# Kernel optimization log

Measured on AMD Instinct MI355X. Metric: run time of the kernel, lower is better.

Reference implementation:

```python
import jax, jax.numpy as jnp
import numpy as np
import math

N_EMBD = 768
N_HEAD = 12
B, T = 4, 1024


def setup_inputs() -> dict:
    key = jax.random.key(0)
    ks = jax.random.split(key, 12)
    s = 0.02
    d = N_EMBD
    inp = {
        'x': jax.random.normal(ks[0], (B, T, d), dtype=jnp.float32),
        'refractory_state': jax.random.uniform(ks[1], (B, T), dtype=jnp.float32),
        'ln1_w': jnp.ones((d,), jnp.float32),
        'ln1_b': jnp.zeros((d,), jnp.float32),
        'c_attn_w': jax.random.normal(ks[2], (d, 3 * d), dtype=jnp.float32) * s,
        'c_attn_b': jnp.zeros((3 * d,), jnp.float32),
        'c_proj_w': jax.random.normal(ks[3], (d, d), dtype=jnp.float32) * s,
        'c_proj_b': jnp.zeros((d,), jnp.float32),
        'threshold': jnp.full((N_HEAD,), 0.01, jnp.float32),
        'leak': jnp.full((N_HEAD,), 2.0, jnp.float32),
        'steepness': jnp.full((N_HEAD,), 2.0, jnp.float32),
        'refractory_strength': jnp.full((N_HEAD,), -2.0, jnp.float32),
        'cross_layer_weight': jnp.full((N_HEAD,), -2.0, jnp.float32),
        'ln2_w': jnp.ones((d,), jnp.float32),
        'ln2_b': jnp.zeros((d,), jnp.float32),
        'fc_w': jax.random.normal(ks[4], (d, 4 * d), dtype=jnp.float32) * s,
        'fc_b': jnp.zeros((4 * d,), jnp.float32),
        'proj_w': jax.random.normal(ks[5], (4 * d, d), dtype=jnp.float32) * s,
        'proj_b': jnp.zeros((d,), jnp.float32),
    }
    return inp


def _layer_norm(x, w, b, eps=1e-5):
    m = jnp.mean(x, axis=-1, keepdims=True)
    v = jnp.var(x, axis=-1, keepdims=True)
    return (x - m) * jax.lax.rsqrt(v + eps) * w + b


def _per_head(p):
    # [H] -> [1, H, 1, 1]
    return p.reshape(1, -1, 1, 1)


def ember_block(x, refractory_state, ln1_w, ln1_b, c_attn_w, c_attn_b,
                c_proj_w, c_proj_b, threshold, leak, steepness,
                refractory_strength, cross_layer_weight,
                ln2_w, ln2_b, fc_w, fc_b, proj_w, proj_b):
    Bx, Tx, C = x.shape
    hd = C // N_HEAD

    h = _layer_norm(x, ln1_w, ln1_b)
    qkv = h @ c_attn_w + c_attn_b
    q, k, v = jnp.split(qkv, 3, axis=-1)
    # [B, T, C] -> [B, H, T, hd]
    q = q.reshape(Bx, Tx, N_HEAD, hd).transpose(0, 2, 1, 3)
    k = k.reshape(Bx, Tx, N_HEAD, hd).transpose(0, 2, 1, 3)
    v = v.reshape(Bx, Tx, N_HEAD, hd).transpose(0, 2, 1, 3)

    att = jnp.einsum('bhqd,bhkd->bhqk', q, k) * (1.0 / math.sqrt(hd))
    causal = jnp.tril(jnp.ones((Tx, Tx), dtype=bool))
    att = jnp.where(causal, att, -jnp.inf)
    att_probs = jax.nn.softmax(att, axis=-1)

    # per-head LIF modulation with refractory dynamics
    thr = jnp.abs(_per_head(threshold)) * 0.1
    lk = jax.nn.sigmoid(_per_head(leak))
    stp = jax.nn.softplus(_per_head(steepness))

    column_load = att_probs.mean(axis=-2, keepdims=True)  # [B,H,1,T]
    ref_strength = jax.nn.softplus(_per_head(refractory_strength))
    eff_thr = thr + ref_strength * column_load
    cross_w = jax.nn.sigmoid(_per_head(cross_layer_weight))
    prev_load = refractory_state[:, None, None, :]  # [B,1,1,T]
    eff_thr = eff_thr + cross_w * prev_load

    fire_mask = jax.nn.sigmoid(stp * (att_probs - eff_thr))
    lif_weights = fire_mask + lk * (1.0 - fire_mask)
    modulated = att_probs * lif_weights
    modulated = modulated / (modulated.sum(axis=-1, keepdims=True) + 1e-8)
    new_refractory = modulated.mean(axis=1).mean(axis=-2)  # [B,T]

    y = jnp.einsum('bhqk,bhkd->bhqd', modulated, v)
    y = y.transpose(0, 2, 1, 3).reshape(Bx, Tx, C)
    y = y @ c_proj_w + c_proj_b
    x = x + y

    # MLP
    h2 = _layer_norm(x, ln2_w, ln2_b)
    h2 = jax.nn.gelu(h2 @ fc_w + fc_b, approximate=False)
    h2 = h2 @ proj_w + proj_b
    x = x + h2
    return x, new_refractory


def reference(x, refractory_state, ln1_w, ln1_b, c_attn_w, c_attn_b,
              c_proj_w, c_proj_b, threshold, leak, steepness,
              refractory_strength, cross_layer_weight,
              ln2_w, ln2_b, fc_w, fc_b, proj_w, proj_b):
    return ember_block(x, refractory_state, ln1_w, ln1_b, c_attn_w, c_attn_b,
                       c_proj_w, c_proj_b, threshold, leak, steepness,
                       refractory_strength, cross_layer_weight,
                       ln2_w, ln2_b, fc_w, fc_b, proj_w, proj_b)
```

## Files before the change

### kernel.cpp

```cpp
#include <hip/hip_runtime.h>
#include <hip/hip_bf16.h>
#include <math.h>

typedef unsigned short ushort;
typedef __attribute__((ext_vector_type(8))) unsigned short ushort8;
typedef __attribute__((ext_vector_type(8))) short s16x8;
typedef __attribute__((ext_vector_type(4))) float f32x4;

constexpr int NE = 768;
constexpr int NH = 12;
constexpr int HD = 64;
constexpr int Bc = 4;
constexpr int Tc = 1024;
constexpr int BT = Bc * Tc;

__device__ __forceinline__ ushort f2bf(float f) {
    __hip_bfloat16 h = __float2bfloat16(f);
    return *reinterpret_cast<ushort*>(&h);
}
__device__ __forceinline__ float bf2f(ushort u) {
    return __uint_as_float(((unsigned)u) << 16);
}
__device__ __forceinline__ float softplus_f(float x) {
    return (x > 20.f) ? x : log1pf(__expf(x));
}
__device__ __forceinline__ float rcp_f(float x) {
#if __has_builtin(__builtin_amdgcn_rcpf)
    return __builtin_amdgcn_rcpf(x);
#else
    return 1.f / x;
#endif
}
__device__ __forceinline__ void gload16(const void* g, void* l) {
    __builtin_amdgcn_global_load_lds((const __attribute__((address_space(1))) void*)g,
                                     (__attribute__((address_space(3))) void*)l, 16, 0, 0);
}

__device__ __forceinline__ void ln_row(const float* __restrict__ x,
                                       const float* __restrict__ w,
                                       const float* __restrict__ b,
                                       ushort* __restrict__ out, int row, int t) {
    const float* xr = x + (size_t)row * NE;
    float v0 = xr[t], v1 = xr[t + 256], v2 = xr[t + 512];
    float s = v0 + v1 + v2;
    float s2 = v0 * v0 + v1 * v1 + v2 * v2;
#pragma unroll
    for (int o = 32; o > 0; o >>= 1) {
        s += __shfl_xor(s, o);
        s2 += __shfl_xor(s2, o);
    }
    __shared__ float lws[4], lws2[4];
    int wv = t >> 6;
    if ((t & 63) == 0) { lws[wv] = s; lws2[wv] = s2; }
    __syncthreads();
    float sum = lws[0] + lws[1] + lws[2] + lws[3];
    float sq = lws2[0] + lws2[1] + lws2[2] + lws2[3];
    float mean = sum * (1.0f / NE);
    float var = sq * (1.0f / NE) - mean * mean;
    float rs = rsqrtf(var + 1e-5f);
    ushort* orow = out + (size_t)row * NE;
    orow[t]       = f2bf((v0 - mean) * rs * w[t]       + b[t]);
    orow[t + 256] = f2bf((v1 - mean) * rs * w[t + 256] + b[t + 256]);
    orow[t + 512] = f2bf((v2 - mean) * rs * w[t + 512] + b[t + 512]);
}

__global__ __launch_bounds__(256) void ln_kernel(const float* __restrict__ x,
                                                 const float* __restrict__ w,
                                                 const float* __restrict__ b,
                                                 ushort* __restrict__ out) {
    ln_row(x, w, b, out, blockIdx.x, threadIdx.x);
}

__device__ __forceinline__ void wconv_tile(const float* __restrict__ W,
                                           ushort* __restrict__ Wt,
                                           int K, int N, int bx, int by, int tid) {
    __shared__ float t[32][33];
    int n0 = bx * 32, k0 = by * 32;
    int c = tid & 31, r4 = tid >> 5;
#pragma unroll
    for (int i = 0; i < 4; ++i) {
        int r = r4 + i * 8;
        t[r][c] = W[(size_t)(k0 + r) * N + n0 + c];
    }
    __syncthreads();
#pragma unroll
    for (int i = 0; i < 4; ++i) {
        int r = r4 + i * 8;
        Wt[(size_t)(n0 + r) * K + k0 + c] = f2bf(t[c][r]);
    }
}

__global__ __launch_bounds__(256) void wconvert_all(
    const float* __restrict__ Wa, ushort* __restrict__ Ta,
    const float* __restrict__ Wc, ushort* __restrict__ Tcp,
    const float* __restrict__ Wf, ushort* __restrict__ Tf,
    const float* __restrict__ Wp, ushort* __restrict__ Tp,
    float* __restrict__ colsum, float* __restrict__ refr_out,
    const float* __restrict__ x, const float* __restrict__ ln1_w,
    const float* __restrict__ ln1_b, ushort* __restrict__ hbuf) {
    int blk = blockIdx.x, tid = threadIdx.x;
    if (blk >= 6964) {
        ln_row(x, ln1_w, ln1_b, hbuf, blk - 6964, tid);
        return;
    }
    if (blk >= 6912) {
        int i = (blk - 6912) * 256 + tid;
        float4 z = make_float4(0.f, 0.f, 0.f, 0.f);
        if (i < 12288) ((float4*)colsum)[i] = z;
        else ((float4*)refr_out)[i - 12288] = z;
        return;
    }
    if (blk < 1728) {
        wconv_tile(Wa, Ta, 768, 2304, blk % 72, blk / 72, tid);
    } else if (blk < 2304) {
        int i = blk - 1728;
        wconv_tile(Wc, Tcp, 768, 768, i % 24, i / 24, tid);
    } else if (blk < 4608) {
        int i = blk - 2304;
        wconv_tile(Wf, Tf, 768, 3072, i % 96, i / 96, tid);
    } else {
        int i = blk - 4608;
        wconv_tile(Wp, Tp, 3072, 768, i % 24, i / 24, tid);
    }
}

template <int BM, int BN, int OUT_MODE, int ACT, bool RES>
__global__ __launch_bounds__(256) void mfma_gemm(
    const ushort* __restrict__ A, const ushort* __restrict__ Bt,
    const float* __restrict__ bias, const float* __restrict__ residual,
    float* __restrict__ Cf, ushort* __restrict__ Cb,
    ushort* __restrict__ Qo, ushort* __restrict__ Ko, ushort* __restrict__ Vo,
    int M, int N, int K, int NBX, int KLD, int NSPLIT) {
    constexpr int NF = (BM == 128) ? 4 : 2;
    constexpr int MF = (BM == 64 && BN == 64) ? 2 : 4;
    constexpr int WN = BN / (NF * 16);
    constexpr int APASS = BM / 32, BPASS = BN / 32;
    constexpr bool DBUF = (BM == 64 && BN == 64);
    constexpr int NBUF = DBUF ? 2 : 1;
    __shared__ __align__(16) ushort As[NBUF * BM * 64];
    __shared__ __align__(16) ushort Bs[NBUF * BN * 64];
    int tid = threadIdx.x;
    int lane = tid & 63;
    int nb = gridDim.x;
    int lin = blockIdx.x;
    int nl = (lin & 7) * (nb >> 3) + (lin >> 3);
    int nper = nb / NSPLIT;
    int sp = nl / nper;
    int rem2 = nl - sp * nper;
    int bx = rem2 % NBX, by = rem2 / NBX;
    int m0 = by * BM, n0 = bx * BN;
    int kbase = sp * K;
    int wave = tid >> 6;
    int wr = wave / WN, wc = wave % WN;
    f32x4 acc[MF][NF] = {};
    int srow = tid >> 3;
    int scol = (tid & 7) ^ (srow & 7);
    const ushort* ga = A + (size_t)(m0 + srow) * KLD + kbase + scol * 8;
    const ushort* gb = Bt + (size_t)(n0 + srow) * KLD + kbase + scol * 8;
    char* lA = (char*)As + tid * 16;
    char* lB = (char*)Bs + tid * 16;
    int fr = lane & 15, g = lane >> 4;
    unsigned swz = (unsigned)((fr & 7) << 4);
    const char* abase = (const char*)As + (wr * (MF * 16) + fr) * 128;
    const char* bbase = (const char*)Bs + (wc * (NF * 16) + fr) * 128;

    if constexpr (DBUF) {
        constexpr int ABYTES = BM * 64 * 2, BBYTES = BN * 64 * 2;
        int nk = K >> 6;
#pragma unroll
        for (int p = 0; p < APASS; ++p) gload16(ga + (size_t)(p * 32) * KLD, lA + p * 4096);
#pragma unroll
        for (int p = 0; p < BPASS; ++p) gload16(gb + (size_t)(p * 32) * KLD, lB + p * 4096);
        for (int k = 0; k < nk; ++k) {
            int cur = k & 1;
            if (k + 1 < nk) {
                int nxt = cur ^ 1;
                int k0 = (k + 1) << 6;
#pragma unroll
                for (int p = 0; p < APASS; ++p)
                    gload16(ga + (size_t)(p * 32) * KLD + k0, lA + nxt * ABYTES + p * 4096);
#pragma unroll
                for (int p = 0; p < BPASS; ++p)
                    gload16(gb + (size_t)(p * 32) * KLD + k0, lB + nxt * BBYTES + p * 4096);
                asm volatile("s_waitcnt vmcnt(4)" ::: "memory");
            } else {
                asm volatile("s_waitcnt vmcnt(0)" ::: "memory");
            }
            __builtin_amdgcn_s_barrier();
#pragma unroll
            for (int ks = 0; ks < 2; ++ks) {
                unsigned o = ((unsigned)(g * 16 + ks * 64)) ^ swz;
                s16x8 af[MF], bf[NF];
#pragma unroll
                for (int i = 0; i < MF; ++i)
                    af[i] = *(const s16x8*)(abase + cur * ABYTES + i * 2048 + o);
#pragma unroll
                for (int i = 0; i < NF; ++i)
                    bf[i] = *(const s16x8*)(bbase + cur * BBYTES + i * 2048 + o);
#pragma unroll
                for (int mi = 0; mi < MF; ++mi)
#pragma unroll
                    for (int ni = 0; ni < NF; ++ni)
                        acc[mi][ni] = __builtin_amdgcn_mfma_f32_16x16x32_bf16(af[mi], bf[ni], acc[mi][ni], 0, 0, 0);
            }
            asm volatile("s_waitcnt lgkmcnt(0)" ::: "memory");
            __builtin_amdgcn_s_barrier();
        }
    } else {
        for (int k0 = 0; k0 < K; k0 += 64) {
#pragma unroll
            for (int p = 0; p < APASS; ++p)
                gload16(ga + (size_t)(p * 32) * KLD + k0, lA + p * 4096);
#pragma unroll
            for (int p = 0; p < BPASS; ++p)
                gload16(gb + (size_t)(p * 32) * KLD + k0, lB + p * 4096);
            __syncthreads();
#pragma unroll
            for (int ks = 0; ks < 2; ++ks) {
                unsigned o = ((unsigned)(g * 16 + ks * 64)) ^ swz;
                s16x8 af[MF], bf[NF];
#pragma unroll
                for (int i = 0; i < MF; ++i) af[i] = *(const s16x8*)(abase + i * 2048 + o);
#pragma unroll
                for (int i = 0; i < NF; ++i) bf[i] = *(const s16x8*)(bbase + i * 2048 + o);
#pragma unroll
                for (int mi = 0; mi < MF; ++mi)
#pragma unroll
                    for (int ni = 0; ni < NF; ++ni)
                        acc[mi][ni] = __builtin_amdgcn_mfma_f32_16x16x32_bf16(af[mi], bf[ni], acc[mi][ni], 0, 0, 0);
            }
            __syncthreads();
        }
    }
#pragma unroll
    for (int mi = 0; mi < MF; ++mi) {
#pragma unroll
        for (int ni = 0; ni < NF; ++ni) {
#pragma unroll
            for (int j = 0; j < 4; ++j) {
                int row = m0 + wr * (MF * 16) + mi * 16 + g * 4 + j;
                int col = n0 + wc * (NF * 16) + ni * 16 + fr;
                float v = acc[mi][ni][j];
                if (OUT_MODE != 3) v += bias[col];
                else if (sp == 0) v += bias[col];
                if (ACT == 1) v = 0.5f * v * (1.0f + erff(v * 0.70710678118654752f));
                if (RES) v += residual[(size_t)row * N + col];
                if (OUT_MODE == 0) {
                    Cf[(size_t)row * N + col] = v;
                } else if (OUT_MODE == 1) {
                    Cb[(size_t)row * N + col] = f2bf(v);
                } else if (OUT_MODE == 3) {
                    atomicAdd(&Cf[(size_t)row * N + col], v);
                } else {
                    int which = col >= 1536 ? 2 : (col >= 768 ? 1 : 0);
                    int rem = col - which * 768;
                    int hh = rem >> 6, d = rem & 63;
                    int b_ = row >> 10, t_ = row & 1023;
                    if (which == 2)
                        Vo[((size_t)(b_ * NH + hh) * HD + d) * Tc + t_] = f2bf(v);
                    else {
                        ushort* dst = which == 0 ? Qo : Ko;
                        dst[((size_t)(b_ * NH + hh) * Tc + t_) * HD + d] = f2bf(v);
                    }
                }
            }
        }
    }
}


__global__ __launch_bounds__(128) void attn_P(
    const ushort* __restrict__ Qp, const ushort* __restrict__ Kp,
    ushort* __restrict__ Pbuf, float* __restrict__ denom, float* __restrict__ colsum) {
    int beta = blockIdx.x;
    int tq = 63 - beta / 48;
    int bh = beta % 48;
    int tid = threadIdx.x;
    int kh = tid >> 6, lane = tid & 63, qlane = lane & 15, g = lane >> 4;
    __shared__ ushort plds[2][16][48];
    __shared__ float cs[1056];
    __shared__ float dden[2][16];
    int nst = (tq + 2) >> 1;
    int smid = (nst + 1) >> 1;
    int slo = kh ? smid : 0, shi = kh ? nst : smid;
    int kmaxc = (tq + 1) * 16;
    for (int i = tid; i < 1056; i += 128) cs[i] = 0.f;
    const ushort* Qb = Qp + (size_t)bh * Tc * HD;
    const ushort* Kb = Kp + (size_t)bh * Tc * HD;
    const ushort* qr = Qb + (size_t)(tq * 16 + qlane) * HD + g * 8;
    s16x8 qf0 = *(const s16x8*)qr;
    s16x8 qf1 = *(const s16x8*)(qr + 32);
    ushort* panel = Pbuf + ((size_t)bh * 1056 + (unsigned)(((tq + 1) * (tq + 1)) >> 2)) * 512;
    int q = tq * 16 + qlane;
    s16x8 preg[16];
    float dpart = 0.f;
#pragma unroll
    for (int ss = 0; ss < 16; ++ss) {
        int s = slo + ss;
        if (s < shi) {
            int kt0 = 2 * s, kt1 = 2 * s + 1;
            {
                const ushort* kr = Kb + (size_t)(kt0 * 16 + qlane) * HD + g * 8;
                s16x8 kf0 = *(const s16x8*)kr;
                s16x8 kf1 = *(const s16x8*)(kr + 32);
                f32x4 z = {0.f, 0.f, 0.f, 0.f};
                z = __builtin_amdgcn_mfma_f32_16x16x32_bf16(kf0, qf0, z, 0, 0, 0);
                z = __builtin_amdgcn_mfma_f32_16x16x32_bf16(kf1, qf1, z, 0, 0, 0);
#pragma unroll
                for (int j = 0; j < 4; ++j) {
                    int key = kt0 * 16 + g * 4 + j;
                    float p = (key <= q) ? __expf(z[j] * 0.125f - 8.f) : 0.f;
                    dpart += p;
                    plds[kh][qlane][g * 4 + j] = f2bf(p);
                }
            }
            if (kt1 <= tq) {
                const ushort* kr = Kb + (size_t)(kt1 * 16 + qlane) * HD + g * 8;
                s16x8 kf0 = *(const s16x8*)kr;
                s16x8 kf1 = *(const s16x8*)(kr + 32);
                f32x4 z = {0.f, 0.f, 0.f, 0.f};
                z = __builtin_amdgcn_mfma_f32_16x16x32_bf16(kf0, qf0, z, 0, 0, 0);
                z = __builtin_amdgcn_mfma_f32_16x16x32_bf16(kf1, qf1, z, 0, 0, 0);
#pragma unroll
                for (int j = 0; j < 4; ++j) {
                    int key = kt1 * 16 + g * 4 + j;
                    float p = (key <= q) ? __expf(z[j] * 0.125f - 8.f) : 0.f;
                    dpart += p;
                    plds[kh][qlane][16 + g * 4 + j] = f2bf(p);
                }
            } else {
#pragma unroll
                for (int j = 0; j < 4; ++j) plds[kh][qlane][16 + g * 4 + j] = 0;
            }
            s16x8 pa = *(const s16x8*)&plds[kh][qlane][g * 8];
            preg[ss] = pa;
            *(s16x8*)(panel + (size_t)s * 512 + lane * 8) = pa;
        }
    }
    dpart += __shfl_xor(dpart, 16);
    dpart += __shfl_xor(dpart, 32);
    if (lane < 16) dden[kh][lane] = dpart;
    __syncthreads();
    float dsum = dden[0][qlane] + dden[1][qlane];
    if (tid < 16) denom[(size_t)bh * Tc + tq * 16 + tid] = dden[0][tid] + dden[1][tid];
    float dinvq = rcp_f(dsum);
#pragma unroll
    for (int ss = 0; ss < 16; ++ss) {
        int s = slo + ss;
        if (s < shi) {
            s16x8 v8 = preg[ss];
            int k0 = s * 32 + g * 8;
#pragma unroll
            for (int j = 0; j < 8; ++j) {
                float r = bf2f((ushort)v8[j]) * dinvq;
                r += __shfl_xor(r, 1);
                r += __shfl_xor(r, 2);
                r += __shfl_xor(r, 4);
                r += __shfl_xor(r, 8);
                if (qlane == 0) cs[k0 + j] += r;
            }
        }
    }
    __syncthreads();
    for (int i = tid; i < kmaxc; i += 128)
        atomicAdd(&colsum[(size_t)bh * Tc + i], cs[i]);
}

__global__ __launch_bounds__(128) void attn_CD(
    const ushort* __restrict__ Pbuf, const ushort* __restrict__ Vt,
    const float* __restrict__ denom, const float* __restrict__ colsum,
    const float* __restrict__ refr_in,
    const float* __restrict__ threshold, const float* __restrict__ leak,
    const float* __restrict__ steepness, const float* __restrict__ refr_strength,
    const float* __restrict__ cross_w,
    ushort* __restrict__ ybuf, float* __restrict__ refr_out) {
    int beta = blockIdx.x;
    int tq = 63 - beta / 48;
    int bh = beta % 48;
    int b = bh / NH, h = bh - b * NH;
    int tid = threadIdx.x;
    int kh = tid >> 6, lane = tid & 63, qlane = lane & 15, g = lane >> 4;
    __shared__ float eff[1056];
    __shared__ float cs[1056];
    __shared__ float msum[2][16];
    __shared__ float minvL[16];
    __shared__ float ymrg[16][68];
    int nst = (tq + 2) >> 1;
    int smid = (nst + 1) >> 1;
    int slo = kh ? smid : 0, shi = kh ? nst : smid;
    int kmaxc = (tq + 1) * 16;
    float thr = fabsf(threshold[h]) * 0.1f;
    float lk = 1.f / (1.f + __expf(-leak[h]));
    float lk1m = 1.f - lk;
    float stp = softplus_f(steepness[h]);
    float rfs = softplus_f(refr_strength[h]);
    float crw = 1.f / (1.f + __expf(-cross_w[h]));
    for (int i = tid; i < 1056; i += 128) {
        eff[i] = (i < kmaxc)
                     ? thr + rfs * (colsum[(size_t)bh * Tc + i] * (1.f / 1024.f))
                           + crw * refr_in[(size_t)b * Tc + i]
                     : 0.f;
        cs[i] = 0.f;
    }
    float dinvq = rcp_f(denom[(size_t)bh * Tc + tq * 16 + qlane]);
    __syncthreads();
    const ushort* panel =
        Pbuf + ((size_t)bh * 1056 + (unsigned)(((tq + 1) * (tq + 1)) >> 2)) * 512;
    s16x8 ptreg[16];
    float msp = 0.f;
#pragma unroll
    for (int ss = 0; ss < 16; ++ss) {
        int s = slo + ss;
        if (s < shi) {
            s16x8 v8 = *(const s16x8*)(panel + (size_t)s * 512 + lane * 8);
            int k0 = s * 32 + g * 8;
            s16x8 pw;
#pragma unroll
            for (int j = 0; j < 8; ++j) {
                float p = bf2f((ushort)v8[j]) * dinvq;
                float fire = rcp_f(1.f + __expf(-stp * (p - eff[k0 + j])));
                float pt = p * (lk + lk1m * fire);
                msp += pt;
                pw[j] = (short)f2bf(pt);
            }
            ptreg[ss] = pw;
        }
    }
    msp += __shfl_xor(msp, 16);
    msp += __shfl_xor(msp, 32);
    if (lane < 16) msum[kh][lane] = msp;
    __syncthreads();
    if (tid < 16) minvL[tid] = rcp_f(msum[0][tid] + msum[1][tid] + 1e-8f);
    __syncthreads();
    float minvq = minvL[qlane];
    const ushort* Vh = Vt + (size_t)bh * HD * Tc;
    f32x4 accY[4] = {};
#pragma unroll
    for (int ss = 0; ss < 16; ++ss) {
        int s = slo + ss;
        if (s < shi) {
            s16x8 pa = ptreg[ss];
            int k0 = s * 32 + g * 8;
#pragma unroll
            for (int j = 0; j < 8; ++j) {
                float r = bf2f((ushort)pa[j]) * minvq;
                r += __shfl_xor(r, 1);
                r += __shfl_xor(r, 2);
                r += __shfl_xor(r, 4);
                r += __shfl_xor(r, 8);
                if (qlane == 0) cs[k0 + j] += r;
            }
#pragma unroll
            for (int dt = 0; dt < 4; ++dt) {
                const ushort* vp = Vh + (size_t)(dt * 16 + qlane) * Tc + s * 32 + g * 8;
                s16x8 vf = *(const s16x8*)vp;
                accY[dt] = __builtin_amdgcn_mfma_f32_16x16x32_bf16(pa, vf, accY[dt], 0, 0, 0);
            }
        }
    }
    if (kh == 1) {
#pragma unroll
        for (int dt = 0; dt < 4; ++dt)
#pragma unroll
            for (int j = 0; j < 4; ++j)
                ymrg[g * 4 + j][dt * 16 + qlane] = accY[dt][j];
    }
    __syncthreads();
    if (kh == 0) {
#pragma unroll
        for (int dt = 0; dt < 4; ++dt)
#pragma unroll
            for (int j = 0; j < 4; ++j) {
                float y = (accY[dt][j] + ymrg[g * 4 + j][dt * 16 + qlane]) * minvL[g * 4 + j];
                ybuf[(size_t)(b * Tc + tq * 16 + g * 4 + j) * NE + h * 64 + dt * 16 + qlane] =
                    f2bf(y);
            }
    }
    for (int i = tid; i < kmaxc; i += 128)
        atomicAdd(&refr_out[(size_t)b * Tc + i], cs[i] * (1.f / (NH * Tc)));
}

extern "C" void kernel_launch(void* const* d_in, const int* in_sizes, int n_in,
                              void* d_out, int out_size, void* d_ws, size_t ws_size,
                              hipStream_t stream) {
    const float* x        = (const float*)d_in[0];
    const float* refr     = (const float*)d_in[1];
    const float* ln1_w    = (const float*)d_in[2];
    const float* ln1_b    = (const float*)d_in[3];
    const float* c_attn_w = (const float*)d_in[4];
    const float* c_attn_b = (const float*)d_in[5];
    const float* c_proj_w = (const float*)d_in[6];
    const float* c_proj_b = (const float*)d_in[7];
    const float* threshold = (const float*)d_in[8];
    const float* leak      = (const float*)d_in[9];
    const float* steepness = (const float*)d_in[10];
    const float* refractory_strength = (const float*)d_in[11];
    const float* cross_layer_weight  = (const float*)d_in[12];
    const float* ln2_w    = (const float*)d_in[13];
    const float* ln2_b    = (const float*)d_in[14];
    const float* fc_w     = (const float*)d_in[15];
    const float* fc_b     = (const float*)d_in[16];
    const float* proj_w   = (const float*)d_in[17];
    const float* proj_b   = (const float*)d_in[18];

    char* ws = (char*)d_ws;
    ushort* hbuf   = (ushort*)(ws + 0);
    ushort* qb     = (ushort*)(ws + 6291456);
    ushort* kb     = (ushort*)(ws + 12582912);
    ushort* vtg    = (ushort*)(ws + 18874368);
    ushort* ybuf   = (ushort*)(ws + 25165824);
    ushort* fc_act = (ushort*)(ws + 6291456);
    float*  denomb = (float*)(ws + 31457280);
    float*  colsum = (float*)(ws + 31653888);
    ushort* wt_attn  = (ushort*)(ws + 31850496);
    ushort* wt_cproj = (ushort*)(ws + 35389440);
    ushort* wt_fc    = (ushort*)(ws + 36569088);
    ushort* wt_proj  = (ushort*)(ws + 41287680);
    ushort* Pbuf     = (ushort*)(ws + 46006272);

    float* xout = (float*)d_out;
    float* refr_out = xout + (size_t)BT * NE;

    wconvert_all<<<11060, 256, 0, stream>>>(c_attn_w, wt_attn, c_proj_w, wt_cproj,
                                            fc_w, wt_fc, proj_w, wt_proj,
                                            colsum, refr_out, x, ln1_w, ln1_b, hbuf);

    mfma_gemm<64, 128, 2, 0, false><<<1152, 256, 0, stream>>>(
        hbuf, wt_attn, c_attn_b, nullptr, nullptr, nullptr, qb, kb, vtg,
        BT, 3 * NE, NE, 18, NE, 1);

    attn_P<<<48 * 64, 128, 0, stream>>>(qb, kb, Pbuf, denomb, colsum);
    attn_CD<<<48 * 64, 128, 0, stream>>>(
        Pbuf, vtg, denomb, colsum, refr, threshold, leak, steepness,
        refractory_strength, cross_layer_weight, ybuf, refr_out);

    mfma_gemm<64, 64, 0, 0, true><<<768, 256, 0, stream>>>(
        ybuf, wt_cproj, c_proj_b, x, xout, nullptr, nullptr, nullptr, nullptr,
        BT, NE, NE, 12, NE, 1);

    ln_kernel<<<BT, 256, 0, stream>>>(xout, ln2_w, ln2_b, hbuf);

    mfma_gemm<128, 128, 1, 1, false><<<768, 256, 0, stream>>>(
        hbuf, wt_fc, fc_b, nullptr, nullptr, fc_act, nullptr, nullptr, nullptr,
        BT, 4 * NE, NE, 24, NE, 1);

    mfma_gemm<64, 64, 0, 0, true><<<768, 256, 0, stream>>>(
        fc_act, wt_proj, proj_b, xout, xout, nullptr, nullptr, nullptr, nullptr,
        BT, NE, 4 * NE, 12, 4 * NE, 1);
}
```

Baseline: 239.0 us.

## Drop register-cached probability panels and recompute from global panel buffer

```diff
diff --git a/kernel.cpp b/kernel.cpp
--- a/kernel.cpp
+++ b/kernel.cpp
@@ -292,50 +292,44 @@
     s16x8 qf1 = *(const s16x8*)(qr + 32);
     ushort* panel = Pbuf + ((size_t)bh * 1056 + (unsigned)(((tq + 1) * (tq + 1)) >> 2)) * 512;
     int q = tq * 16 + qlane;
-    s16x8 preg[16];
     float dpart = 0.f;
-#pragma unroll
-    for (int ss = 0; ss < 16; ++ss) {
-        int s = slo + ss;
-        if (s < shi) {
-            int kt0 = 2 * s, kt1 = 2 * s + 1;
-            {
-                const ushort* kr = Kb + (size_t)(kt0 * 16 + qlane) * HD + g * 8;
-                s16x8 kf0 = *(const s16x8*)kr;
-                s16x8 kf1 = *(const s16x8*)(kr + 32);
-                f32x4 z = {0.f, 0.f, 0.f, 0.f};
-                z = __builtin_amdgcn_mfma_f32_16x16x32_bf16(kf0, qf0, z, 0, 0, 0);
-                z = __builtin_amdgcn_mfma_f32_16x16x32_bf16(kf1, qf1, z, 0, 0, 0);
-#pragma unroll
-                for (int j = 0; j < 4; ++j) {
-                    int key = kt0 * 16 + g * 4 + j;
-                    float p = (key <= q) ? __expf(z[j] * 0.125f - 8.f) : 0.f;
-                    dpart += p;
-                    plds[kh][qlane][g * 4 + j] = f2bf(p);
-                }
-            }
-            if (kt1 <= tq) {
-                const ushort* kr = Kb + (size_t)(kt1 * 16 + qlane) * HD + g * 8;
-                s16x8 kf0 = *(const s16x8*)kr;
-                s16x8 kf1 = *(const s16x8*)(kr + 32);
-                f32x4 z = {0.f, 0.f, 0.f, 0.f};
-                z = __builtin_amdgcn_mfma_f32_16x16x32_bf16(kf0, qf0, z, 0, 0, 0);
-                z = __builtin_amdgcn_mfma_f32_16x16x32_bf16(kf1, qf1, z, 0, 0, 0);
-#pragma unroll
-                for (int j = 0; j < 4; ++j) {
-                    int key = kt1 * 16 + g * 4 + j;
-                    float p = (key <= q) ? __expf(z[j] * 0.125f - 8.f) : 0.f;
-                    dpart += p;
-                    plds[kh][qlane][16 + g * 4 + j] = f2bf(p);
-                }
-            } else {
-#pragma unroll
-                for (int j = 0; j < 4; ++j) plds[kh][qlane][16 + g * 4 + j] = 0;
-            }
-            s16x8 pa = *(const s16x8*)&plds[kh][qlane][g * 8];
-            preg[ss] = pa;
-            *(s16x8*)(panel + (size_t)s * 512 + lane * 8) = pa;
-        }
+    for (int s = slo; s < shi; ++s) {
+        int kt0 = 2 * s, kt1 = 2 * s + 1;
+        {
+            const ushort* kr = Kb + (size_t)(kt0 * 16 + qlane) * HD + g * 8;
+            s16x8 kf0 = *(const s16x8*)kr;
+            s16x8 kf1 = *(const s16x8*)(kr + 32);
+            f32x4 z = {0.f, 0.f, 0.f, 0.f};
+            z = __builtin_amdgcn_mfma_f32_16x16x32_bf16(kf0, qf0, z, 0, 0, 0);
+            z = __builtin_amdgcn_mfma_f32_16x16x32_bf16(kf1, qf1, z, 0, 0, 0);
+#pragma unroll
+            for (int j = 0; j < 4; ++j) {
+                int key = kt0 * 16 + g * 4 + j;
+                float p = (key <= q) ? __expf(z[j] * 0.125f - 8.f) : 0.f;
+                dpart += p;
+                plds[kh][qlane][g * 4 + j] = f2bf(p);
+            }
+        }
+        if (kt1 <= tq) {
+            const ushort* kr = Kb + (size_t)(kt1 * 16 + qlane) * HD + g * 8;
+            s16x8 kf0 = *(const s16x8*)kr;
+            s16x8 kf1 = *(const s16x8*)(kr + 32);
+            f32x4 z = {0.f, 0.f, 0.f, 0.f};
+            z = __builtin_amdgcn_mfma_f32_16x16x32_bf16(kf0, qf0, z, 0, 0, 0);
+            z = __builtin_amdgcn_mfma_f32_16x16x32_bf16(kf1, qf1, z, 0, 0, 0);
+#pragma unroll
+            for (int j = 0; j < 4; ++j) {
+                int key = kt1 * 16 + g * 4 + j;
+                float p = (key <= q) ? __expf(z[j] * 0.125f - 8.f) : 0.f;
+                dpart += p;
+                plds[kh][qlane][16 + g * 4 + j] = f2bf(p);
+            }
+        } else {
+#pragma unroll
+            for (int j = 0; j < 4; ++j) plds[kh][qlane][16 + g * 4 + j] = 0;
+        }
+        s16x8 pa = *(const s16x8*)&plds[kh][qlane][g * 8];
+        *(s16x8*)(panel + (size_t)s * 512 + lane * 8) = pa;
     }
     dpart += __shfl_xor(dpart, 16);
     dpart += __shfl_xor(dpart, 32);
@@ -344,21 +338,17 @@
     float dsum = dden[0][qlane] + dden[1][qlane];
     if (tid < 16) denom[(size_t)bh * Tc + tq * 16 + tid] = dden[0][tid] + dden[1][tid];
     float dinvq = rcp_f(dsum);
-#pragma unroll
-    for (int ss = 0; ss < 16; ++ss) {
-        int s = slo + ss;
-        if (s < shi) {
-            s16x8 v8 = preg[ss];
-            int k0 = s * 32 + g * 8;
-#pragma unroll
-            for (int j = 0; j < 8; ++j) {
-                float r = bf2f((ushort)v8[j]) * dinvq;
-                r += __shfl_xor(r, 1);
-                r += __shfl_xor(r, 2);
-                r += __shfl_xor(r, 4);
-                r += __shfl_xor(r, 8);
-                if (qlane == 0) cs[k0 + j] += r;
-            }
+    for (int s = slo; s < shi; ++s) {
+        s16x8 v8 = *(const s16x8*)(panel + (size_t)s * 512 + lane * 8);
+        int k0 = s * 32 + g * 8;
+#pragma unroll
+        for (int j = 0; j < 8; ++j) {
+            float r = bf2f((ushort)v8[j]) * dinvq;
+            r += __shfl_xor(r, 1);
+            r += __shfl_xor(r, 2);
+            r += __shfl_xor(r, 4);
+            r += __shfl_xor(r, 8);
+            if (qlane == 0) cs[k0 + j] += r;
         }
     }
     __syncthreads();
@@ -381,10 +371,9 @@
     int tid = threadIdx.x;
     int kh = tid >> 6, lane = tid & 63, qlane = lane & 15, g = lane >> 4;
     __shared__ float eff[1056];
-    __shared__ float cs[1056];
+    __shared__ float u[1056];
     __shared__ float msum[2][16];
     __shared__ float minvL[16];
-    __shared__ float ymrg[16][68];
     int nst = (tq + 2) >> 1;
     int smid = (nst + 1) >> 1;
     int slo = kh ? smid : 0, shi = kh ? nst : smid;
@@ -400,30 +389,21 @@
                      ? thr + rfs * (colsum[(size_t)bh * Tc + i] * (1.f / 1024.f))
                            + crw * refr_in[(size_t)b * Tc + i]
                      : 0.f;
-        cs[i] = 0.f;
+        u[i] = 0.f;
     }
     float dinvq = rcp_f(denom[(size_t)bh * Tc + tq * 16 + qlane]);
     __syncthreads();
     const ushort* panel =
         Pbuf + ((size_t)bh * 1056 + (unsigned)(((tq + 1) * (tq + 1)) >> 2)) * 512;
-    s16x8 ptreg[16];
     float msp = 0.f;
-#pragma unroll
-    for (int ss = 0; ss < 16; ++ss) {
-        int s = slo + ss;
-        if (s < shi) {
-            s16x8 v8 = *(const s16x8*)(panel + (size_t)s * 512 + lane * 8);
-            int k0 = s * 32 + g * 8;
-            s16x8 pw;
-#pragma unroll
-            for (int j = 0; j < 8; ++j) {
-                float p = bf2f((ushort)v8[j]) * dinvq;
-                float fire = rcp_f(1.f + __expf(-stp * (p - eff[k0 + j])));
-                float pt = p * (lk + lk1m * fire);
-                msp += pt;
-                pw[j] = (short)f2bf(pt);
-            }
-            ptreg[ss] = pw;
+    for (int s = slo; s < shi; ++s) {
+        s16x8 v8 = *(const s16x8*)(panel + (size_t)s * 512 + lane * 8);
+        int k0 = s * 32 + g * 8;
+#pragma unroll
+        for (int j = 0; j < 8; ++j) {
+            float p = bf2f((ushort)v8[j]) * dinvq;
+            float fire = rcp_f(1.f + __expf(-stp * (p - eff[k0 + j])));
+            msp += p * (lk + lk1m * fire);
         }
     }
     msp += __shfl_xor(msp, 16);
@@ -435,35 +415,40 @@
     float minvq = minvL[qlane];
     const ushort* Vh = Vt + (size_t)bh * HD * Tc;
     f32x4 accY[4] = {};
-#pragma unroll
-    for (int ss = 0; ss < 16; ++ss) {
-        int s = slo + ss;
-        if (s < shi) {
-            s16x8 pa = ptreg[ss];
-            int k0 = s * 32 + g * 8;
-#pragma unroll
-            for (int j = 0; j < 8; ++j) {
-                float r = bf2f((ushort)pa[j]) * minvq;
-                r += __shfl_xor(r, 1);
-                r += __shfl_xor(r, 2);
-                r += __shfl_xor(r, 4);
-                r += __shfl_xor(r, 8);
-                if (qlane == 0) cs[k0 + j] += r;
-            }
-#pragma unroll
-            for (int dt = 0; dt < 4; ++dt) {
-                const ushort* vp = Vh + (size_t)(dt * 16 + qlane) * Tc + s * 32 + g * 8;
-                s16x8 vf = *(const s16x8*)vp;
-                accY[dt] = __builtin_amdgcn_mfma_f32_16x16x32_bf16(pa, vf, accY[dt], 0, 0, 0);
-            }
-        }
-    }
+    for (int s = slo; s < shi; ++s) {
+        s16x8 v8 = *(const s16x8*)(panel + (size_t)s * 512 + lane * 8);
+        int k0 = s * 32 + g * 8;
+        s16x8 pa;
+#pragma unroll
+        for (int j = 0; j < 8; ++j) {
+            float p = bf2f((ushort)v8[j]) * dinvq;
+            float fire = rcp_f(1.f + __expf(-stp * (p - eff[k0 + j])));
+            float pt = p * (lk + lk1m * fire);
+            pa[j] = (short)f2bf(pt);
+            float r = pt * minvq;
+            r += __shfl_xor(r, 1);
+            r += __shfl_xor(r, 2);
+            r += __shfl_xor(r, 4);
+            r += __shfl_xor(r, 8);
+            if (qlane == 0) u[k0 + j] += r;
+        }
+#pragma unroll
+        for (int dt = 0; dt < 4; ++dt) {
+            const ushort* vp = Vh + (size_t)(dt * 16 + qlane) * Tc + s * 32 + g * 8;
+            s16x8 vf = *(const s16x8*)vp;
+            accY[dt] = __builtin_amdgcn_mfma_f32_16x16x32_bf16(pa, vf, accY[dt], 0, 0, 0);
+        }
+    }
+    __syncthreads();
+    for (int i = tid; i < kmaxc; i += 128)
+        atomicAdd(&refr_out[(size_t)b * Tc + i], u[i] * (1.f / (NH * Tc)));
+    __syncthreads();
     if (kh == 1) {
 #pragma unroll
         for (int dt = 0; dt < 4; ++dt)
 #pragma unroll
             for (int j = 0; j < 4; ++j)
-                ymrg[g * 4 + j][dt * 16 + qlane] = accY[dt][j];
+                u[(g * 4 + j) * 66 + dt * 16 + qlane] = accY[dt][j];
     }
     __syncthreads();
     if (kh == 0) {
@@ -471,13 +456,12 @@
         for (int dt = 0; dt < 4; ++dt)
 #pragma unroll
             for (int j = 0; j < 4; ++j) {
-                float y = (accY[dt][j] + ymrg[g * 4 + j][dt * 16 + qlane]) * minvL[g * 4 + j];
+                float y = (accY[dt][j] + u[(g * 4 + j) * 66 + dt * 16 + qlane]) *
+                          minvL[g * 4 + j];
                 ybuf[(size_t)(b * Tc + tq * 16 + g * 4 + j) * NE + h * 64 + dt * 16 + qlane] =
                     f2bf(y);
             }
     }
-    for (int i = tid; i < kmaxc; i += 128)
-        atomicAdd(&refr_out[(size_t)b * Tc + i], cs[i] * (1.f / (NH * Tc)));
 }
 
 extern "C" void kernel_launch(void* const* d_in, const int* in_sizes, int n_in,
```

Result: no change. 240.4 us (+0.6%).
